# Optimization experiments

Measured on AMD Instinct MI355X. Metric: run time of the kernel, lower is better.

## Reference

```python
import math
import jax, jax.numpy as jnp
import numpy as np

N_TOKENS = 32768
N_TYPES = 21
D_MODEL = 1024
N_SEQS = 64


def setup_inputs() -> dict:
    key = jax.random.key(0)
    k1, k2, k3, k4 = jax.random.split(key, 4)
    x = jax.random.normal(k1, (N_TOKENS, N_TYPES), dtype=jnp.float32)
    # nn.Linear(n_types, d_model): weight [d_model, n_types], bias [d_model]
    W = jax.random.normal(k2, (D_MODEL, N_TYPES), dtype=jnp.float32) / math.sqrt(N_TYPES)
    b = jax.random.normal(k3, (D_MODEL,), dtype=jnp.float32) * 0.01
    # sorted segment ids -> ragged batch of N_SEQS sequences
    batch = jnp.sort(jax.random.randint(k4, (N_TOKENS,), 0, N_SEQS, dtype=jnp.int64))
    return {"x": x, "W": W, "b": b, "batch": batch}


def _position_encoding(max_len, d_model, dtype):
    pos = jnp.arange(max_len, dtype=jnp.float32)[:, None]          # [L,1]
    div = jnp.exp(jnp.arange(0, d_model, 2, dtype=jnp.float32) * (-math.log(10000.0) / d_model))
    ang = pos * div                                                 # [L, d/2]
    pe = jnp.zeros((max_len, d_model), dtype=jnp.float32)
    pe = pe.at[:, 0::2].set(jnp.sin(ang)).at[:, 1::2].set(jnp.cos(ang))
    return pe.astype(dtype)


def reference(x, W, b, batch):
    d_model = W.shape[0]
    # Linear projection + sqrt(d_model) scale
    h = (jnp.einsum('nt,dt->nd', x, W) + b) * math.sqrt(d_model)    # [N, d_model]

    # pad_batch: relabel via unique ids, compute per-token position within its
    # sequence, and scatter into a padded [n_seqs, max_len, d_model] tensor.
    bnp = np.asarray(batch)
    _, inv, counts = np.unique(bnp, return_inverse=True, return_counts=True)
    n_seqs = counts.shape[0]
    max_len = int(counts.max())
    offsets = np.concatenate([np.zeros(1, dtype=np.int64), np.cumsum(counts)[:-1]])
    pos = np.arange(bnp.shape[0], dtype=np.int64) - offsets[inv]    # position within sequence

    padded = jnp.zeros((n_seqs, max_len, d_model), dtype=h.dtype)
    padded = padded.at[jnp.asarray(inv), jnp.asarray(pos)].set(h)

    # mask: True where valid token (original returns ~pad_mask)
    mask = jnp.arange(max_len)[None, :] < jnp.asarray(counts)[:, None]

    pe = _position_encoding(max_len, d_model, h.dtype)              # [L, d_model]
    out = padded + pe[None, :, :]
    return (out, mask)
```

## Files before the change

kernel.cpp:

```cpp
#include <hip/hip_runtime.h>
#include <hip/hip_bf16.h>
#include <math.h>

typedef float f4 __attribute__((ext_vector_type(4)));
typedef float f32x4 __attribute__((ext_vector_type(4)));
typedef short bf16x8 __attribute__((ext_vector_type(8)));

__device__ inline unsigned short f2bf(float f) {
  unsigned int u = __builtin_bit_cast(unsigned int, f);
  unsigned int r = (u + 0x7FFFu + ((u >> 16) & 1u)) >> 16;
  return (unsigned short)r;
}

__global__ __launch_bounds__(256) void setup_kernel(
    const int* __restrict__ batch, int n, const float* __restrict__ W,
    int* __restrict__ tables, unsigned short* __restrict__ wbf) {
  int t = threadIdx.x;

  if (blockIdx.x != 0) {
    int r = (blockIdx.x - 1) * 256 + t;
    const float* wr = W + r * 21;
    unsigned short* wo = wbf + r * 32;
#pragma unroll
    for (int k = 0; k < 21; ++k) wo[k] = f2bf(wr[k]);
#pragma unroll
    for (int k = 21; k < 32; ++k) wo[k] = 0;
    return;
  }

  __shared__ int samp[256];
  __shared__ int csum[64];
  __shared__ int fine[64];
  __shared__ int sbase[64];
  __shared__ int lbs[65];
  __shared__ int stride_s;
  if (t == 0) stride_s = (batch[n - 1] == 0) ? 2 : 1;
  if (t < 64) { csum[t] = 0; fine[t] = 0; }
  __syncthreads();
  int stride = stride_s;
  int window = (n + 255) >> 8;
  {
    long long idx = (long long)t * window;
    if (idx > n - 1) idx = n - 1;
    samp[t] = batch[idx * stride];
  }
  __syncthreads();
  {
    int v = t >> 2, q = t & 3;
    int c = 0;
#pragma unroll
    for (int i = 0; i < 64; ++i) c += (samp[q * 64 + i] < v) ? 1 : 0;
    atomicAdd(&csum[v], c);
  }
  __syncthreads();
  if (t < 64) {
    int c = csum[t];
    sbase[t] = (c == 0) ? 0 : (c - 1) * window;
  }
  __syncthreads();
  {
    int v = t >> 2, q = t & 3;
    int wpt = (window + 3) >> 2;
    int S = sbase[v];
    int c = 0;
    for (int j = q * wpt; j < (q + 1) * wpt && j < window; ++j) {
      int idx = S + j;
      if (idx < n && batch[(size_t)idx * stride] < v) c++;
    }
    atomicAdd(&fine[v], c);
  }
  __syncthreads();
  if (t < 64) {
    lbs[t] = sbase[t] + fine[t];
    if (t == 0) lbs[64] = n;
  }
  __syncthreads();
  if (t < 64) {
    int cnt = lbs[t + 1] - lbs[t];
    unsigned long long present = __ballot(cnt > 0);
    int seg = __popcll(present & ((1ull << t) - 1ull));
    int nseq = __popcll(present);
    if (cnt > 0) { tables[seg] = lbs[t]; tables[64 + seg] = cnt; }
    if (t >= nseq) { tables[t] = 0; tables[64 + t] = 0; }
  }
}

__global__ __launch_bounds__(256) void embed_kernel(
    const float* __restrict__ x, const unsigned short* __restrict__ wb,
    const float* __restrict__ bias, const int* __restrict__ tables,
    float* __restrict__ out, float* __restrict__ mask,
    int L, int n_tokens) {
  int t = threadIdx.x;
  int lane = t & 63;
  int wv = t >> 6;
  int g = lane >> 4, c = lane & 15;

  int stripe = blockIdx.x >> 2;
  int colGroup = blockIdx.x & 3;
  int base = stripe * 16;

  int s0 = base / L;
  int s0L = s0 * L;
  int Lnext = s0L + L;

  int row_r = base + c;
  int inc_r = (row_r >= Lnext) ? 1 : 0;
  int p_r = row_r - (inc_r ? Lnext : s0L);
  int cnt_r = tables[64 + s0 + inc_r];
  unsigned long long bal = __ballot(p_r < cnt_r);
  unsigned int m16 = (unsigned int)(bal & 0xFFFFull);
  int rank_r = __popc(m16 & ((1u << c) - 1u));

  int p0 = base - s0L;
  int cnt0 = tables[64 + s0];
  int tok0 = tables[s0] + (p0 < cnt0 ? p0 : cnt0);
  int tok = tok0 + rank_r;
  if (tok > n_tokens - 1) tok = n_tokens - 1;

  const float* xr = x + tok * 21;
  float vv[8];
#pragma unroll
  for (int j = 0; j < 8; ++j) vv[j] = 0.f;
  if (g == 0) {
#pragma unroll
    for (int j = 0; j < 8; ++j) vv[j] = xr[j];
  } else if (g == 1) {
#pragma unroll
    for (int j = 0; j < 8; ++j) vv[j] = xr[8 + j];
  } else if (g == 2) {
#pragma unroll
    for (int j = 0; j < 5; ++j) vv[j] = xr[16 + j];
  }
  bf16x8 af;
#pragma unroll
  for (int j = 0; j < 8; ++j) af[j] = (short)f2bf(vv[j]);

  int prow[4], pval[4];
#pragma unroll
  for (int j = 0; j < 4; ++j) {
    int rr = 4 * g + j;
    int row = base + rr;
    int inc = (row >= Lnext) ? 1 : 0;
    prow[j] = row - (inc ? Lnext : s0L);
    pval[j] = (m16 >> rr) & 1;
  }

  const float KC = -0.01798894603901599f;
  int cb = colGroup * 256 + wv * 64;
  bool isOdd = (c & 1) != 0;

#pragma unroll
  for (int ct = 0; ct < 4; ++ct) {
    int col = cb + ct * 16 + c;
    bf16x8 bfrag = *(const bf16x8*)(wb + col * 32 + 8 * g);
    f32x4 acc = {0.f, 0.f, 0.f, 0.f};
    acc = __builtin_amdgcn_mfma_f32_16x16x32_bf16(af, bfrag, acc, 0, 0, 0);
    float bv = bias[col];
    float dv = __expf(KC * (float)(col >> 1));
#pragma unroll
    for (int j = 0; j < 4; ++j) {
      float ang = (float)prow[j] * dv;
      float pe = isOdd ? __cosf(ang) : __sinf(ang);
      float res = pval[j] ? fmaf(acc[j] + bv, 32.f, pe) : pe;
      out[(size_t)(base + 4 * g + j) * 1024 + col] = res;
    }
  }

  if (colGroup == 0 && t < 16)
    mask[base + t] = ((m16 >> t) & 1) ? 1.0f : 0.0f;
}

extern "C" void kernel_launch(void* const* d_in, const int* in_sizes, int n_in,
                              void* d_out, int out_size, void* d_ws, size_t ws_size,
                              hipStream_t stream) {
  const float* x = (const float*)d_in[0];
  const float* W = (const float*)d_in[1];
  const float* b = (const float*)d_in[2];
  const int* batch = (const int*)d_in[3];
  int n_tokens = in_sizes[3];
  float* out = (float*)d_out;

  int L = out_size / (64 * 1025);
  int totalRows = 64 * L;

  int* tables = (int*)d_ws;
  unsigned short* wbf = (unsigned short*)((char*)d_ws + 1024);

  setup_kernel<<<5, 256, 0, stream>>>(batch, n_tokens, W, tables, wbf);

  int stripes = totalRows / 16;
  embed_kernel<<<stripes * 4, 256, 0, stream>>>(x, wbf, b, tables, out,
                                                out + (size_t)totalRows * 1024,
                                                L, n_tokens);
}
```

Measured before the change: 40.55 us.

## Make embed kernel persistent over stripes, hoisting weight, bias and frequency loads

The embed kernel now launches a fixed grid of 2048 blocks, and each block loops over stripes in a grid-stride pattern. The per-column weight fragments, bias values and exp-based frequencies are loaded and computed once per block instead of once per stripe. This cuts redundant global loads, exp work and block launch overhead. In exchange it reduces parallelism slack and adds loop overhead and register pressure.

```diff
diff --git a/kernel.cpp b/kernel.cpp
--- a/kernel.cpp
+++ b/kernel.cpp
@@ -89,85 +89,94 @@
     const float* __restrict__ x, const unsigned short* __restrict__ wb,
     const float* __restrict__ bias, const int* __restrict__ tables,
     float* __restrict__ out, float* __restrict__ mask,
-    int L, int n_tokens) {
+    int L, int n_tokens, int stripes, int blocksPerCG) {
   int t = threadIdx.x;
   int lane = t & 63;
   int wv = t >> 6;
   int g = lane >> 4, c = lane & 15;
 
-  int stripe = blockIdx.x >> 2;
-  int colGroup = blockIdx.x & 3;
-  int base = stripe * 16;
-
-  int s0 = base / L;
-  int s0L = s0 * L;
-  int Lnext = s0L + L;
-
-  int row_r = base + c;
-  int inc_r = (row_r >= Lnext) ? 1 : 0;
-  int p_r = row_r - (inc_r ? Lnext : s0L);
-  int cnt_r = tables[64 + s0 + inc_r];
-  unsigned long long bal = __ballot(p_r < cnt_r);
-  unsigned int m16 = (unsigned int)(bal & 0xFFFFull);
-  int rank_r = __popc(m16 & ((1u << c) - 1u));
-
-  int p0 = base - s0L;
-  int cnt0 = tables[64 + s0];
-  int tok0 = tables[s0] + (p0 < cnt0 ? p0 : cnt0);
-  int tok = tok0 + rank_r;
-  if (tok > n_tokens - 1) tok = n_tokens - 1;
-
-  const float* xr = x + tok * 21;
-  float vv[8];
-#pragma unroll
-  for (int j = 0; j < 8; ++j) vv[j] = 0.f;
-  if (g == 0) {
-#pragma unroll
-    for (int j = 0; j < 8; ++j) vv[j] = xr[j];
-  } else if (g == 1) {
-#pragma unroll
-    for (int j = 0; j < 8; ++j) vv[j] = xr[8 + j];
-  } else if (g == 2) {
-#pragma unroll
-    for (int j = 0; j < 5; ++j) vv[j] = xr[16 + j];
-  }
-  bf16x8 af;
-#pragma unroll
-  for (int j = 0; j < 8; ++j) af[j] = (short)f2bf(vv[j]);
-
-  int prow[4], pval[4];
-#pragma unroll
-  for (int j = 0; j < 4; ++j) {
-    int rr = 4 * g + j;
-    int row = base + rr;
-    int inc = (row >= Lnext) ? 1 : 0;
-    prow[j] = row - (inc ? Lnext : s0L);
-    pval[j] = (m16 >> rr) & 1;
-  }
+  int cg = blockIdx.x & 3;
+  int sb = blockIdx.x >> 2;
 
   const float KC = -0.01798894603901599f;
-  int cb = colGroup * 256 + wv * 64;
-  bool isOdd = (c & 1) != 0;
-
+  int cb = cg * 256 + wv * 64;
+  bf16x8 wfr[4];
+  float bv[4], dv[4];
 #pragma unroll
   for (int ct = 0; ct < 4; ++ct) {
     int col = cb + ct * 16 + c;
-    bf16x8 bfrag = *(const bf16x8*)(wb + col * 32 + 8 * g);
-    f32x4 acc = {0.f, 0.f, 0.f, 0.f};
-    acc = __builtin_amdgcn_mfma_f32_16x16x32_bf16(af, bfrag, acc, 0, 0, 0);
-    float bv = bias[col];
-    float dv = __expf(KC * (float)(col >> 1));
+    wfr[ct] = *(const bf16x8*)(wb + (size_t)col * 32 + 8 * g);
+    bv[ct] = bias[col];
+    dv[ct] = __expf(KC * (float)(col >> 1));
+  }
+  bool isOdd = (c & 1) != 0;
+
+  for (int stripe = sb; stripe < stripes; stripe += blocksPerCG) {
+    int base = stripe * 16;
+
+    int s0 = base / L;
+    int s0L = s0 * L;
+    int Lnext = s0L + L;
+
+    int row_r = base + c;
+    int inc_r = (row_r >= Lnext) ? 1 : 0;
+    int p_r = row_r - (inc_r ? Lnext : s0L);
+    int cnt_r = tables[64 + s0 + inc_r];
+    unsigned long long bal = __ballot(p_r < cnt_r);
+    unsigned int m16 = (unsigned int)(bal & 0xFFFFull);
+    int rank_r = __popc(m16 & ((1u << c) - 1u));
+
+    int p0 = base - s0L;
+    int cnt0 = tables[64 + s0];
+    int tok0 = tables[s0] + (p0 < cnt0 ? p0 : cnt0);
+    int tok = tok0 + rank_r;
+    if (tok > n_tokens - 1) tok = n_tokens - 1;
+
+    const float* xr = x + (size_t)tok * 21;
+    float vv[8];
+#pragma unroll
+    for (int j = 0; j < 8; ++j) vv[j] = 0.f;
+    if (g == 0) {
+#pragma unroll
+      for (int j = 0; j < 8; ++j) vv[j] = xr[j];
+    } else if (g == 1) {
+#pragma unroll
+      for (int j = 0; j < 8; ++j) vv[j] = xr[8 + j];
+    } else if (g == 2) {
+#pragma unroll
+      for (int j = 0; j < 5; ++j) vv[j] = xr[16 + j];
+    }
+    bf16x8 af;
+#pragma unroll
+    for (int j = 0; j < 8; ++j) af[j] = (short)f2bf(vv[j]);
+
+    int prow[4], pval[4];
 #pragma unroll
     for (int j = 0; j < 4; ++j) {
-      float ang = (float)prow[j] * dv;
-      float pe = isOdd ? __cosf(ang) : __sinf(ang);
-      float res = pval[j] ? fmaf(acc[j] + bv, 32.f, pe) : pe;
-      out[(size_t)(base + 4 * g + j) * 1024 + col] = res;
-    }
-  }
-
-  if (colGroup == 0 && t < 16)
-    mask[base + t] = ((m16 >> t) & 1) ? 1.0f : 0.0f;
+      int rr = 4 * g + j;
+      int row = base + rr;
+      int inc = (row >= Lnext) ? 1 : 0;
+      prow[j] = row - (inc ? Lnext : s0L);
+      pval[j] = (m16 >> rr) & 1;
+    }
+
+#pragma unroll
+    for (int ct = 0; ct < 4; ++ct) {
+      int col = cb + ct * 16 + c;
+      f32x4 acc = {0.f, 0.f, 0.f, 0.f};
+      acc = __builtin_amdgcn_mfma_f32_16x16x32_bf16(af, wfr[ct], acc, 0, 0, 0);
+#pragma unroll
+      for (int j = 0; j < 4; ++j) {
+        float ang = (float)prow[j] * dv[ct];
+        float pe = isOdd ? __cosf(ang) : __sinf(ang);
+        float res = pval[j] ? fmaf(acc[j] + bv[ct], 32.f, pe) : pe;
+        out[(size_t)(base + 4 * g + j) * 1024 + col] = res;
+      }
+    }
+
+    if (cg == 0 && t < 16)
+      mask[base + t] = ((m16 >> t) & 1) ? 1.0f : 0.0f;
+  }
 }
 
 extern "C" void kernel_launch(void* const* d_in, const int* in_sizes, int n_in,
@@ -189,7 +198,9 @@
   setup_kernel<<<5, 256, 0, stream>>>(batch, n_tokens, W, tables, wbf);
 
   int stripes = totalRows / 16;
-  embed_kernel<<<stripes * 4, 256, 0, stream>>>(x, wbf, b, tables, out,
-                                                out + (size_t)totalRows * 1024,
-                                                L, n_tokens);
-}
+  int blocksPerCG = 512;
+  if (blocksPerCG > stripes) blocksPerCG = stripes;
+  embed_kernel<<<blocksPerCG * 4, 256, 0, stream>>>(
+      x, wbf, b, tables, out, out + (size_t)totalRows * 1024,
+      L, n_tokens, stripes, blocksPerCG);
+}
```

Result: slower. 42.33 us (+4.4%).
